# Performance work log

Hardware: AMD Instinct MI355X
Metric: run time of the kernel (lower is better)

## Reference

```python
import jax, jax.numpy as jnp
import numpy as np


def setup_inputs() -> dict:
    key = jax.random.key(0)
    k1, k2, k3 = jax.random.split(key, 3)
    B, T, H, OUT = 32, 2048, 1024, 256
    hidden_states = jax.random.normal(k1, (B, T, H), dtype=jnp.float32)
    W1 = jax.random.normal(k2, (H, H), dtype=jnp.float32) * (1.0 / np.sqrt(H))
    b1 = jnp.zeros((H,), dtype=jnp.float32)
    Wv = jax.random.normal(k3, (2 * H, OUT), dtype=jnp.float32) * (1.0 / np.sqrt(2 * H))
    bv = jnp.zeros((OUT,), dtype=jnp.float32)
    return {"hidden_states": hidden_states, "W1": W1, "b1": b1, "Wv": Wv, "bv": bv}


def reference(hidden_states, W1, b1, Wv, bv):
    # first_score = Dense(H)(hidden_states): [B,T,H]
    first_score = jnp.einsum('bth,hk->btk', hidden_states, W1) + b1
    # h_t = last timestep of the PROJECTED states: [B,H]
    h_t = first_score[:, -1, :]
    # score = dot([first_score, h_t], [2,1]): [B,T]
    score = jnp.einsum('bth,bh->bt', first_score, h_t)
    attention_weights = jax.nn.softmax(score, axis=-1)  # softmax over T
    # context = dot([hidden_states, weights], [1,1]): contract T -> [B,H]
    context_vector = jnp.einsum('bth,bt->bh', hidden_states, attention_weights)
    pre_activation = jnp.concatenate([context_vector, h_t], axis=-1)  # [B,2H]
    return jnp.tanh(pre_activation @ Wv + bv)  # [B,256]
```

## Files before the change

### kernel.cpp

```cpp
#include <hip/hip_runtime.h>
#include <math.h>

#define B   32
#define T   2048
#define H   1024
#define OUTD 256
#define NC  32
#define KC1 16

__global__ __launch_bounds__(256) void k1a_partial_ht(
    const float* __restrict__ hs, const float* __restrict__ W1,
    float* __restrict__ ph)
{
    const int tid = threadIdx.x;
    const int h   = blockIdx.x * 256 + tid;
    const int k0  = blockIdx.y * 64;

    __shared__ float s_hs[B][64];
    for (int it = 0; it < 8; ++it) {
        int idx = tid + it * 256;
        int b = idx >> 6, k = idx & 63;
        s_hs[b][k] = hs[((size_t)(b * T + (T - 1)) << 10) + k0 + k];
    }
    __syncthreads();

    float acc[B];
#pragma unroll
    for (int b = 0; b < B; ++b) acc[b] = 0.f;

    for (int k4 = 0; k4 < 16; ++k4) {
        float w0 = W1[(size_t)(k0 + k4 * 4 + 0) * H + h];
        float w1 = W1[(size_t)(k0 + k4 * 4 + 1) * H + h];
        float w2 = W1[(size_t)(k0 + k4 * 4 + 2) * H + h];
        float w3 = W1[(size_t)(k0 + k4 * 4 + 3) * H + h];
#pragma unroll
        for (int b = 0; b < B; ++b) {
            const float4 hv = *(const float4*)&s_hs[b][k4 * 4];
            acc[b] = fmaf(hv.x, w0, acc[b]);
            acc[b] = fmaf(hv.y, w1, acc[b]);
            acc[b] = fmaf(hv.z, w2, acc[b]);
            acc[b] = fmaf(hv.w, w3, acc[b]);
        }
    }
    float* dst = ph + ((size_t)blockIdx.y * B << 10);
#pragma unroll
    for (int b = 0; b < B; ++b) dst[((size_t)b << 10) + h] = acc[b];
}

__global__ __launch_bounds__(256) void k1b_reduce_ht(
    const float* __restrict__ ph, const float* __restrict__ b1,
    float* __restrict__ h_t)
{
    int i = blockIdx.x * 256 + threadIdx.x;
    int h = i & (H - 1);
    float s = b1[h];
#pragma unroll
    for (int c = 0; c < KC1; ++c)
        s += ph[((size_t)c * B << 10) + i];
    h_t[i] = s;
}

__global__ __launch_bounds__(256) void k2_compute_u(
    const float* __restrict__ W1, const float* __restrict__ h_t,
    float* __restrict__ u)
{
    const int wid  = threadIdx.x >> 6;
    const int lane = threadIdx.x & 63;
    const int k    = blockIdx.x * 4 + wid;
    const float4* wr = (const float4*)(W1 + ((size_t)k << 10));
    float4 wq[4];
#pragma unroll
    for (int j = 0; j < 4; ++j) wq[j] = wr[lane + 64 * j];

    for (int b = 0; b < B; ++b) {
        const float4* hr = (const float4*)(h_t + ((size_t)b << 10));
        float s = 0.f;
#pragma unroll
        for (int j = 0; j < 4; ++j) {
            float4 hv = hr[lane + 64 * j];
            s += wq[j].x * hv.x + wq[j].y * hv.y + wq[j].z * hv.z + wq[j].w * hv.w;
        }
#pragma unroll
        for (int off = 32; off; off >>= 1) s += __shfl_xor(s, off, 64);
        if (lane == 0) u[((size_t)b << 10) + k] = s;
    }
}

__global__ __launch_bounds__(256) void k3_fused(
    const float* __restrict__ hs, const float* __restrict__ u,
    float* __restrict__ ctx_p, float* __restrict__ m_p, float* __restrict__ l_p)
{
    const int c    = blockIdx.x;
    const int b    = blockIdx.y;
    const int w    = threadIdx.x >> 6;
    const int lane = threadIdx.x & 63;
    const int tid  = threadIdx.x;

    const float4* urow = (const float4*)(u + ((size_t)b << 10));
    float4 uq[4];
#pragma unroll
    for (int j = 0; j < 4; ++j) uq[j] = urow[lane + 64 * j];

    const int t0 = c * 64 + w * 16;
    const float4* xrow = (const float4*)(hs + ((size_t)(b * T + t0) << 10));

    float m = -INFINITY, lsum = 0.f;
    float4 acc[4];
#pragma unroll
    for (int j = 0; j < 4; ++j) acc[j] = make_float4(0.f, 0.f, 0.f, 0.f);

    float4 x[4], y[4];
#pragma unroll
    for (int j = 0; j < 4; ++j) x[j] = xrow[lane + 64 * j];

    for (int r = 0; r < 16; ++r) {
        const float4* nrow = xrow + 256;
        if (r < 15) {
#pragma unroll
            for (int j = 0; j < 4; ++j) y[j] = nrow[lane + 64 * j];
        }
        float s = 0.f;
#pragma unroll
        for (int j = 0; j < 4; ++j)
            s += x[j].x * uq[j].x + x[j].y * uq[j].y + x[j].z * uq[j].z + x[j].w * uq[j].w;
#pragma unroll
        for (int off = 32; off; off >>= 1) s += __shfl_xor(s, off, 64);

        float mn = fmaxf(m, s);
        float al = __expf(m - mn);
        float wt = __expf(s - mn);
        lsum = lsum * al + wt;
#pragma unroll
        for (int j = 0; j < 4; ++j) {
            acc[j].x = fmaf(acc[j].x, al, wt * x[j].x);
            acc[j].y = fmaf(acc[j].y, al, wt * x[j].y);
            acc[j].z = fmaf(acc[j].z, al, wt * x[j].z);
            acc[j].w = fmaf(acc[j].w, al, wt * x[j].w);
        }
        m = mn;
#pragma unroll
        for (int j = 0; j < 4; ++j) x[j] = y[j];
        xrow = nrow;
    }

    __shared__ float sm[4], sl[4];
    __shared__ float sacc[4][H];
    if (lane == 0) { sm[w] = m; sl[w] = lsum; }
    __syncthreads();
    const float mp = fmaxf(fmaxf(sm[0], sm[1]), fmaxf(sm[2], sm[3]));
    const float alw = __expf(m - mp);
    float4* sa = (float4*)&sacc[w][0];
#pragma unroll
    for (int j = 0; j < 4; ++j) {
        float4 v;
        v.x = acc[j].x * alw; v.y = acc[j].y * alw;
        v.z = acc[j].z * alw; v.w = acc[j].w * alw;
        sa[lane + 64 * j] = v;
    }
    __syncthreads();
    float lp = 0.f;
#pragma unroll
    for (int ww = 0; ww < 4; ++ww) lp += sl[ww] * __expf(sm[ww] - mp);

    float* dst = ctx_p + (((size_t)b * NC + c) << 10);
#pragma unroll
    for (int i = 0; i < 4; ++i) {
        int h = tid + 256 * i;
        dst[h] = sacc[0][h] + sacc[1][h] + sacc[2][h] + sacc[3][h];
    }
    if (tid == 0) { m_p[b * NC + c] = mp; l_p[b * NC + c] = lp; }
}

__global__ __launch_bounds__(256) void k4_combine(
    const float* __restrict__ ctx_p, const float* __restrict__ m_p,
    const float* __restrict__ l_p, const float* __restrict__ h_t,
    float* __restrict__ pre)
{
    const int b   = blockIdx.x;
    const int tid = threadIdx.x;
    __shared__ float e[NC];
    float M = -INFINITY;
    for (int c = 0; c < NC; ++c) M = fmaxf(M, m_p[b * NC + c]);
    float L = 0.f;
    for (int c = 0; c < NC; ++c) L += l_p[b * NC + c] * __expf(m_p[b * NC + c] - M);
    if (tid < NC) e[tid] = __expf(m_p[b * NC + tid] - M);
    __syncthreads();
    const float inv = 1.f / L;
#pragma unroll
    for (int i = 0; i < 4; ++i) {
        int h = tid + 256 * i;
        float s = 0.f;
#pragma unroll
        for (int c = 0; c < NC; ++c)
            s += ctx_p[(((size_t)b * NC + c) << 10) + h] * e[c];
        pre[((size_t)b << 11) + h] = s * inv;
        pre[((size_t)b << 11) + H + h] = h_t[((size_t)b << 10) + h];
    }
}

__global__ __launch_bounds__(256) void k5a_matmul(
    const float* __restrict__ pre, const float* __restrict__ Wv,
    float* __restrict__ accum)
{
    const int kc = blockIdx.x;
    const int b  = blockIdx.y;
    const int o  = threadIdx.x;
    __shared__ float sp[256];
    sp[o] = pre[((size_t)b << 11) + kc * 256 + o];
    __syncthreads();
    float acc = 0.f;
    const float* wv = Wv + (size_t)kc * 256 * OUTD + o;
#pragma unroll 8
    for (int k = 0; k < 256; ++k)
        acc = fmaf(sp[k], wv[(size_t)k * OUTD], acc);
    atomicAdd(&accum[b * OUTD + o], acc);
}

__global__ __launch_bounds__(256) void k5b_tanh(
    const float* __restrict__ accum, const float* __restrict__ bv,
    float* __restrict__ out)
{
    int i = blockIdx.x * 256 + threadIdx.x;
    out[i] = tanhf(accum[i] + bv[i & (OUTD - 1)]);
}

extern "C" void kernel_launch(void* const* d_in, const int* in_sizes, int n_in,
                              void* d_out, int out_size, void* d_ws, size_t ws_size,
                              hipStream_t stream)
{
    const float* hs = (const float*)d_in[0];
    const float* W1 = (const float*)d_in[1];
    const float* b1 = (const float*)d_in[2];
    const float* Wv = (const float*)d_in[3];
    const float* bv = (const float*)d_in[4];
    float* out = (float*)d_out;
    float* ws  = (float*)d_ws;

    float* ph    = ws;
    float* h_t   = ph + (size_t)KC1 * B * H;
    float* u     = h_t + (size_t)B * H;
    float* m_p   = u + (size_t)B * H;
    float* l_p   = m_p + B * NC;
    float* ctx_p = l_p + B * NC;
    float* pre   = ctx_p + (size_t)B * NC * H;
    float* accum = pre + (size_t)B * 2 * H;

    hipMemsetAsync(accum, 0, B * OUTD * sizeof(float), stream);

    k1a_partial_ht<<<dim3(4, KC1), 256, 0, stream>>>(hs, W1, ph);
    k1b_reduce_ht<<<(B * H) / 256, 256, 0, stream>>>(ph, b1, h_t);
    k2_compute_u<<<H / 4, 256, 0, stream>>>(W1, h_t, u);
    k3_fused<<<dim3(NC, B), 256, 0, stream>>>(hs, u, ctx_p, m_p, l_p);
    k4_combine<<<B, 256, 0, stream>>>(ctx_p, m_p, l_p, h_t, pre);
    k5a_matmul<<<dim3(8, B), 256, 0, stream>>>(pre, Wv, accum);
    k5b_tanh<<<B, 256, 0, stream>>>(accum, bv, out);
}
```

Baseline: 436.5 us.

## Fuse softmax combine, output matmul and tanh into one kernel

Merges the combine, output projection and tanh kernels into a single 1024-thread-per-batch kernel. The concatenated pre-activation stays in shared memory and the four K-slices are reduced in shared memory instead of with global atomics. This removes two launches, the memset, and the pre/accum round trips. In exchange it uses only 32 blocks for the Wv matmul, so each block streams all of Wv with less parallelism than the previous 8x32 grid.

```diff
diff --git a/kernel.cpp b/kernel.cpp
--- a/kernel.cpp
+++ b/kernel.cpp
@@ -171,57 +171,53 @@
     if (tid == 0) { m_p[b * NC + c] = mp; l_p[b * NC + c] = lp; }
 }
 
-__global__ __launch_bounds__(256) void k4_combine(
+__global__ __launch_bounds__(1024) void k45_out(
     const float* __restrict__ ctx_p, const float* __restrict__ m_p,
     const float* __restrict__ l_p, const float* __restrict__ h_t,
-    float* __restrict__ pre)
+    const float* __restrict__ Wv, const float* __restrict__ bv,
+    float* __restrict__ out)
 {
     const int b   = blockIdx.x;
     const int tid = threadIdx.x;
+    __shared__ float sp[2 * H];
     __shared__ float e[NC];
+    __shared__ float red[1024];
+
     float M = -INFINITY;
+#pragma unroll
     for (int c = 0; c < NC; ++c) M = fmaxf(M, m_p[b * NC + c]);
     float L = 0.f;
+#pragma unroll
     for (int c = 0; c < NC; ++c) L += l_p[b * NC + c] * __expf(m_p[b * NC + c] - M);
-    if (tid < NC) e[tid] = __expf(m_p[b * NC + tid] - M);
-    __syncthreads();
     const float inv = 1.f / L;
-#pragma unroll
-    for (int i = 0; i < 4; ++i) {
-        int h = tid + 256 * i;
+    if (tid < NC) e[tid] = __expf(m_p[b * NC + tid] - M) * inv;
+    __syncthreads();
+
+    {
+        const int h = tid;
         float s = 0.f;
 #pragma unroll
         for (int c = 0; c < NC; ++c)
             s += ctx_p[(((size_t)b * NC + c) << 10) + h] * e[c];
-        pre[((size_t)b << 11) + h] = s * inv;
-        pre[((size_t)b << 11) + H + h] = h_t[((size_t)b << 10) + h];
-    }
-}
-
-__global__ __launch_bounds__(256) void k5a_matmul(
-    const float* __restrict__ pre, const float* __restrict__ Wv,
-    float* __restrict__ accum)
-{
-    const int kc = blockIdx.x;
-    const int b  = blockIdx.y;
-    const int o  = threadIdx.x;
-    __shared__ float sp[256];
-    sp[o] = pre[((size_t)b << 11) + kc * 256 + o];
-    __syncthreads();
+        sp[h]     = s;
+        sp[H + h] = h_t[((size_t)b << 10) + h];
+    }
+    __syncthreads();
+
+    const int o = tid & (OUTD - 1);
+    const int q = tid >> 8;
     float acc = 0.f;
-    const float* wv = Wv + (size_t)kc * 256 * OUTD + o;
+    const float* wv = Wv + (size_t)(q * 512) * OUTD + o;
+    const float* s0 = sp + q * 512;
 #pragma unroll 8
-    for (int k = 0; k < 256; ++k)
-        acc = fmaf(sp[k], wv[(size_t)k * OUTD], acc);
-    atomicAdd(&accum[b * OUTD + o], acc);
-}
-
-__global__ __launch_bounds__(256) void k5b_tanh(
-    const float* __restrict__ accum, const float* __restrict__ bv,
-    float* __restrict__ out)
-{
-    int i = blockIdx.x * 256 + threadIdx.x;
-    out[i] = tanhf(accum[i] + bv[i & (OUTD - 1)]);
+    for (int k = 0; k < 512; ++k)
+        acc = fmaf(s0[k], wv[(size_t)k * OUTD], acc);
+    red[tid] = acc;
+    __syncthreads();
+    if (tid < OUTD) {
+        float r = red[tid] + red[tid + 256] + red[tid + 512] + red[tid + 768] + bv[tid];
+        out[b * OUTD + tid] = tanhf(r);
+    }
 }
 
 extern "C" void kernel_launch(void* const* d_in, const int* in_sizes, int n_in,
@@ -242,16 +238,10 @@
     float* m_p   = u + (size_t)B * H;
     float* l_p   = m_p + B * NC;
     float* ctx_p = l_p + B * NC;
-    float* pre   = ctx_p + (size_t)B * NC * H;
-    float* accum = pre + (size_t)B * 2 * H;
-
-    hipMemsetAsync(accum, 0, B * OUTD * sizeof(float), stream);
 
     k1a_partial_ht<<<dim3(4, KC1), 256, 0, stream>>>(hs, W1, ph);
     k1b_reduce_ht<<<(B * H) / 256, 256, 0, stream>>>(ph, b1, h_t);
     k2_compute_u<<<H / 4, 256, 0, stream>>>(W1, h_t, u);
     k3_fused<<<dim3(NC, B), 256, 0, stream>>>(hs, u, ctx_p, m_p, l_p);
-    k4_combine<<<B, 256, 0, stream>>>(ctx_p, m_p, l_p, h_t, pre);
-    k5a_matmul<<<dim3(8, B), 256, 0, stream>>>(pre, Wv, accum);
-    k5b_tanh<<<B, 256, 0, stream>>>(accum, bv, out);
-}
+    k45_out<<<B, 1024, 0, stream>>>(ctx_p, m_p, l_p, h_t, Wv, bv, out);
+}
```

Result: no change. 444.8 us (+1.9%).
